# Kernel tuning notes

Hardware: AMD Instinct MI355X
Metric: run time of the kernel (lower is better)

The kernel has to match this reference:

```python
import jax, jax.numpy as jnp
import numpy as np

MUL0, MUL1 = 32, 16          # multiplicities of 0e and 1o in irreps_node
RBF, HID = 16, 64
O1 = MUL0 * MUL0             # path 0e x 0e -> 0e
O2 = O1 + MUL0 * MUL1        # path 0e x 1o -> 1o
O3 = O2 + MUL1 * MUL1        # path 1o x 0e -> 1o
WNUMEL = O3 + MUL1 * MUL0    # path 1o x 1o -> 0e  => 2304 total
C_PATH = 1.0 / np.sqrt(MUL0 + MUL1).astype(np.float32)  # per-output fan-in norm
C_110 = 1.0 / np.sqrt(3.0)   # CG factor for 1o x 1o -> 0e (component norm)


def setup_inputs() -> dict:
    key = jax.random.key(0)
    ks = jax.random.split(key, 16)
    N, E = 50000, 200000
    x = jax.random.normal(ks[0], (N, MUL0 + 3 * MUL1), jnp.float32)
    edge_src = jax.random.randint(ks[1], (E,), 0, N)
    edge_dst = jax.random.randint(ks[2], (E,), 0, N)
    edge_sh = jax.random.normal(ks[3], (E, 4), jnp.float32)
    edge_rbf = jax.random.uniform(ks[4], (E, RBF), jnp.float32)
    # RadialMLP params (fan-in scaled init)
    w1 = jax.random.normal(ks[5], (RBF, HID), jnp.float32) / np.sqrt(RBF)
    b1 = jnp.zeros((HID,), jnp.float32)
    w2 = jax.random.normal(ks[6], (HID, HID), jnp.float32) / np.sqrt(HID)
    b2 = jnp.zeros((HID,), jnp.float32)
    w3 = jax.random.normal(ks[7], (HID, WNUMEL), jnp.float32) / np.sqrt(HID)
    b3 = jnp.zeros((WNUMEL,), jnp.float32)
    # o3.Linear weights (per-irrep mixing, fan-in normalization folded in)
    ws_self = jax.random.normal(ks[8], (MUL0, MUL0), jnp.float32) / np.sqrt(MUL0)
    wv_self = jax.random.normal(ks[9], (MUL1, MUL1), jnp.float32) / np.sqrt(MUL1)
    ws_out = jax.random.normal(ks[10], (MUL0, MUL0), jnp.float32) / np.sqrt(MUL0)
    wv_out = jax.random.normal(ks[11], (MUL1, MUL1), jnp.float32) / np.sqrt(MUL1)
    return {"x": x, "edge_src": edge_src, "edge_dst": edge_dst,
            "edge_sh": edge_sh, "edge_rbf": edge_rbf,
            "w1": w1, "b1": b1, "w2": w2, "b2": b2, "w3": w3, "b3": b3,
            "ws_self": ws_self, "wv_self": wv_self,
            "ws_out": ws_out, "wv_out": wv_out}


def _irrep_linear(x, ws, wv):
    # per-irrep mixing of '32x0e + 16x1o' features; x: [N, 80]
    n = x.shape[0]
    s = x[:, :MUL0] @ ws                                     # [N, 32]
    v = jnp.einsum('nid,io->nod', x[:, MUL0:].reshape(n, MUL1, 3), wv)
    return jnp.concatenate([s, v.reshape(n, 3 * MUL1)], axis=-1)


def reference(x, edge_src, edge_dst, edge_sh, edge_rbf,
              w1, b1, w2, b2, w3, b3, ws_self, wv_self, ws_out, wv_out):
    N = x.shape[0]
    E = edge_rbf.shape[0]
    # radial MLP -> per-edge TP weights [E, 2304]
    h = jax.nn.silu(edge_rbf @ w1 + b1)
    h = jax.nn.silu(h @ w2 + b2)
    W = h @ w3 + b3
    W1 = W[:, :O1].reshape(E, MUL0, MUL0)      # 0e x 0e -> 0e
    W2 = W[:, O1:O2].reshape(E, MUL0, MUL1)    # 0e x 1o -> 1o
    W3 = W[:, O2:O3].reshape(E, MUL1, MUL1)    # 1o x 0e -> 1o
    W4 = W[:, O3:].reshape(E, MUL1, MUL0)      # 1o x 1o -> 0e
    # gather source node features per edge
    xs = x[edge_src, :MUL0]                                   # [E, 32]
    xv = x[edge_src, MUL0:].reshape(E, MUL1, 3)               # [E, 16, 3]
    sh_s = edge_sh[:, 0]                                      # [E]
    sh_v = edge_sh[:, 1:4]                                    # [E, 3]
    # CG tensor product paths
    out_s = jnp.einsum('ei,eio->eo', xs * sh_s[:, None], W1)
    out_s = out_s + C_110 * jnp.einsum('eid,ed,eio->eo', xv, sh_v, W4)
    out_v = jnp.einsum('ei,ed,eio->eod', xs, sh_v, W2)
    out_v = out_v + jnp.einsum('eid,eio->eod', xv * sh_s[:, None, None], W3)
    m = C_PATH * jnp.concatenate([out_s, out_v.reshape(E, 3 * MUL1)], axis=-1)
    # scatter-add + degree normalize
    agg = jax.ops.segment_sum(m, edge_dst, num_segments=N)
    deg = jax.ops.segment_sum(jnp.ones((E,), x.dtype), edge_dst, num_segments=N)
    agg = agg / jnp.maximum(deg, 1.0)[:, None]
    return _irrep_linear(x, ws_self, wv_self) + _irrep_linear(agg, ws_out, wv_out)
```

## Files before the change

### kernel.cpp

```cpp
#include <hip/hip_runtime.h>
#include <math.h>

#define MUL0    32
#define MUL1    16
#define RBFD    16
#define HIDD    64
#define OFF1    1024
#define OFF2    1536
#define OFF3    1792
#define WNUMEL  2304
#define FDIM    80
#define CPATH   0.14433756729740643f
#define C110    0.57735026918962576f

#define TE       160
#define NTHREADS 320
#define NCT      144

#define W3B_ELEMS (NCT*2*64*8)
#define W1B_ELEMS (4*64*8)
#define W2B_ELEMS (4*2*64*8)

typedef float          f32x4   __attribute__((ext_vector_type(4)));
typedef short          short8  __attribute__((ext_vector_type(8)));
typedef short          short4v __attribute__((ext_vector_type(4)));
typedef unsigned short u16;

__device__ __forceinline__ float silu(float v) {
    return v / (1.0f + __expf(-v));
}
__device__ __forceinline__ u16 f2bf(float f) {
    unsigned int u = __float_as_uint(f);
    u += 0x7fffu + ((u >> 16) & 1u);
    return (u16)(u >> 16);
}
__device__ __forceinline__ float bf2f(u16 s) {
    return __uint_as_float(((unsigned int)s) << 16);
}
__device__ __forceinline__ f32x4 cvt4(short4v s) {
    f32x4 r;
    r[0] = bf2f((u16)s[0]); r[1] = bf2f((u16)s[1]);
    r[2] = bf2f((u16)s[2]); r[3] = bf2f((u16)s[3]);
    return r;
}
__device__ __forceinline__ f32x4 mfma16(short8 a, short8 b, f32x4 c) {
    return __builtin_amdgcn_mfma_f32_16x16x32_bf16(a, b, c, 0, 0, 0);
}

__global__ void k_prep(const float* __restrict__ w3,
                       const float* __restrict__ w1,
                       const float* __restrict__ w2,
                       u16* __restrict__ w3b,
                       u16* __restrict__ w1b,
                       u16* __restrict__ w2b) {
    int idx = blockIdx.x * 256 + threadIdx.x;
    if (idx < W3B_ELEMS) {
        int j  = idx & 7;
        int l  = (idx >> 3) & 63;
        int kh = (idx >> 9) & 1;
        int ct = idx >> 10;
        int k = kh * 32 + 8 * (l >> 4) + j;
        int c = ct * 16 + (l & 15);
        w3b[idx] = f2bf(w3[k * WNUMEL + c]);
        return;
    }
    idx -= W3B_ELEMS;
    if (idx < W1B_ELEMS) {
        int j  = idx & 7;
        int l  = (idx >> 3) & 63;
        int ct = idx >> 9;
        int k = 8 * (l >> 4) + j;
        int c = ct * 16 + (l & 15);
        w1b[idx] = (k < RBFD) ? f2bf(w1[k * HIDD + c]) : (u16)0;
        return;
    }
    idx -= W1B_ELEMS;
    if (idx < W2B_ELEMS) {
        int j  = idx & 7;
        int l  = (idx >> 3) & 63;
        int kh = (idx >> 9) & 1;
        int ct = idx >> 10;
        int k = kh * 32 + 8 * (l >> 4) + j;
        int c = ct * 16 + (l & 15);
        w2b[idx] = f2bf(w2[k * HIDD + c]);
    }
}

__global__ __launch_bounds__(320)
void k_edge(const float* __restrict__ x,
            const int*   __restrict__ esrc,
            const int*   __restrict__ edst,
            const float* __restrict__ esh,
            const float* __restrict__ erbf,
            const u16*   __restrict__ w1b,
            const float* __restrict__ b1,
            const u16*   __restrict__ w2b,
            const float* __restrict__ b2,
            const u16*   __restrict__ w3b,
            const float* __restrict__ b3,
            float* __restrict__ agg,
            float* __restrict__ deg)
{
    __shared__ alignas(16) unsigned char smem[54016];
    u16*   S     = (u16*)smem;
    float* s_b3  = (float*)(smem + 40960);
    float* s_sh  = (float*)(smem + 50176);
    int*   s_src = (int*)(smem + 52736);
    int*   s_dst = (int*)(smem + 53376);

    const int tid = threadIdx.x;
    const int eb  = blockIdx.x * TE;
    const int w   = tid >> 6;
    const int l   = tid & 63;
    const int lo  = l & 15;
    const int g   = l >> 4;

    if (tid < TE) {
        s_src[tid] = esrc[eb + tid];
        s_dst[tid] = edst[eb + tid];
    }
    for (int idx = tid; idx < TE * 4; idx += NTHREADS)
        s_sh[idx] = esh[eb * 4 + idx];

    float cb1[4], cb2[4];
    #pragma unroll
    for (int ct = 0; ct < 4; ++ct) {
        cb1[ct] = b1[ct * 16 + lo];
        cb2[ct] = b2[ct * 16 + lo];
    }

    const short8* W1B = (const short8*)w1b;
    const short8* W2B = (const short8*)w2b;

    #pragma unroll
    for (int gr = 0; gr < 2; ++gr) {
        const int e0 = 32 * w + 16 * gr;
        short8 ar = {0, 0, 0, 0, 0, 0, 0, 0};
        if (g < 2) {
            const float* rp = erbf + (size_t)(eb + e0 + lo) * RBFD + 8 * g;
            f32x4 r0 = *(const f32x4*)rp;
            f32x4 r1 = *(const f32x4*)(rp + 4);
            ar[0] = f2bf(r0[0]); ar[1] = f2bf(r0[1]);
            ar[2] = f2bf(r0[2]); ar[3] = f2bf(r0[3]);
            ar[4] = f2bf(r1[0]); ar[5] = f2bf(r1[1]);
            ar[6] = f2bf(r1[2]); ar[7] = f2bf(r1[3]);
        }
        #pragma unroll
        for (int ct = 0; ct < 4; ++ct) {
            f32x4 t = {cb1[ct], cb1[ct], cb1[ct], cb1[ct]};
            t = mfma16(ar, W1B[ct * 64 + l], t);
            #pragma unroll
            for (int r = 0; r < 4; ++r)
                S[(e0 + 4 * g + r) * 72 + ct * 16 + lo] = f2bf(silu(t[r]));
        }
    }

    #pragma unroll
    for (int gr = 0; gr < 2; ++gr) {
        const int e0 = 32 * w + 16 * gr;
        short8 a0 = *(const short8*)&S[(e0 + lo) * 72 + 0  + 8 * g];
        short8 a1 = *(const short8*)&S[(e0 + lo) * 72 + 32 + 8 * g];
        #pragma unroll
        for (int ct = 0; ct < 4; ++ct) {
            f32x4 t = {cb2[ct], cb2[ct], cb2[ct], cb2[ct]};
            t = mfma16(a0, W2B[(ct * 2 + 0) * 64 + l], t);
            t = mfma16(a1, W2B[(ct * 2 + 1) * 64 + l], t);
            #pragma unroll
            for (int r = 0; r < 4; ++r)
                S[(e0 + 4 * g + r) * 72 + ct * 16 + lo] = f2bf(silu(t[r]));
        }
    }

    short8 a[2][2];
    #pragma unroll
    for (int rt = 0; rt < 2; ++rt) {
        const int e0 = 32 * w + 16 * rt;
        a[rt][0] = *(const short8*)&S[(e0 + lo) * 72 + 0  + 8 * g];
        a[rt][1] = *(const short8*)&S[(e0 + lo) * 72 + 32 + 8 * g];
    }
    __syncthreads();

    if (tid < TE) {
        const int el = tid, grp = el >> 4, e16 = el & 15;
        const float sh0 = s_sh[el * 4 + 0];
        const float sh1 = s_sh[el * 4 + 1];
        const float sh2 = s_sh[el * 4 + 2];
        const float sh3 = s_sh[el * 4 + 3];
        const float* xrow = x + (size_t)s_src[el] * FDIM;
        u16* fsB = S + grp * 768 + e16;
        u16* xsB = S + 7680  + grp * 512 + e16;
        u16* xvB = S + 12800 + grp * 768 + e16;
        #pragma unroll
        for (int v = 0; v < 8; ++v) {
            f32x4 x4 = *(const f32x4*)(xrow + 4 * v);
            #pragma unroll
            for (int c2 = 0; c2 < 4; ++c2) {
                int i = 4 * v + c2;
                fsB[i * 16] = f2bf(x4[c2] * sh0);
                xsB[i * 16] = f2bf(x4[c2]);
            }
        }
        float buf[48];
        #pragma unroll
        for (int v = 0; v < 12; ++v) {
            f32x4 t4 = *(const f32x4*)(xrow + MUL0 + 4 * v);
            buf[4*v] = t4[0]; buf[4*v+1] = t4[1];
            buf[4*v+2] = t4[2]; buf[4*v+3] = t4[3];
        }
        #pragma unroll
        for (int i = 0; i < 16; ++i) {
            float v0 = buf[3*i], v1 = buf[3*i+1], v2 = buf[3*i+2];
            xvB[(0  + i) * 16] = f2bf(v0 * sh0);
            xvB[(16 + i) * 16] = f2bf(v1 * sh0);
            xvB[(32 + i) * 16] = f2bf(v2 * sh0);
            fsB[(32 + i) * 16] = f2bf(C110 * (v0 * sh1 + v1 * sh2 + v2 * sh3));
        }
    } else {
        for (int idx = tid - TE; idx < WNUMEL; idx += NTHREADS - TE)
            s_b3[idx] = b3[idx];
    }
    __syncthreads();

    const short8* WB = (const short8*)w3b;
    f32x4 acc[2][6];
    #pragma unroll
    for (int rt = 0; rt < 2; ++rt)
        #pragma unroll
        for (int p = 0; p < 6; ++p)
            acc[rt][p] = (f32x4){0.f, 0.f, 0.f, 0.f};

    for (int i = 0; i < 32; ++i) {
        if ((i & 3) == 0 && i) __builtin_amdgcn_s_barrier();
        short8 b0a = WB[(4*i + 0) * 64 + l];
        short8 b0b = WB[(4*i + 1) * 64 + l];
        short8 b1a = WB[(4*i + 2) * 64 + l];
        short8 b1b = WB[(4*i + 3) * 64 + l];
        short8 b2a = WB[(128 + 2*i) * 64 + l];
        short8 b2b = WB[(129 + 2*i) * 64 + l];
        float bs0 = s_b3[(2*i)     * 16 + lo];
        float bs1 = s_b3[(2*i + 1) * 16 + lo];
        float bs2 = s_b3[(64 + i)  * 16 + lo];
        #pragma unroll
        for (int rt = 0; rt < 2; ++rt) {
            const int fb = 2 * w + rt;
            f32x4 t0 = {bs0, bs0, bs0, bs0};
            t0 = mfma16(a[rt][0], b0a, t0); t0 = mfma16(a[rt][1], b0b, t0);
            f32x4 t1 = {bs1, bs1, bs1, bs1};
            t1 = mfma16(a[rt][0], b1a, t1); t1 = mfma16(a[rt][1], b1b, t1);
            f32x4 t2 = {bs2, bs2, bs2, bs2};
            t2 = mfma16(a[rt][0], b2a, t2); t2 = mfma16(a[rt][1], b2b, t2);
            f32x4 f1 = cvt4(*(const short4v*)&S[fb * 768 + i * 16 + 4 * g]);
            f32x4 f2 = cvt4(*(const short4v*)&S[7680 + fb * 512 + i * 16 + 4 * g]);
            acc[rt][0] += f1 * t0;
            acc[rt][1] += f1 * t1;
            acc[rt][2] += f2 * t2;
        }
    }
    for (int i = 0; i < 16; ++i) {
        if ((i & 3) == 0) __builtin_amdgcn_s_barrier();
        short8 b4a0 = WB[(224 + 4*i) * 64 + l];
        short8 b4a1 = WB[(225 + 4*i) * 64 + l];
        short8 b4b0 = WB[(226 + 4*i) * 64 + l];
        short8 b4b1 = WB[(227 + 4*i) * 64 + l];
        short8 b3a  = WB[(192 + 2*i) * 64 + l];
        short8 b3b  = WB[(193 + 2*i) * 64 + l];
        float bs0 = s_b3[(112 + 2*i) * 16 + lo];
        float bs1 = s_b3[(113 + 2*i) * 16 + lo];
        float bs2 = s_b3[(96 + i)    * 16 + lo];
        #pragma unroll
        for (int rt = 0; rt < 2; ++rt) {
            const int fb = 2 * w + rt;
            f32x4 t4a = {bs0, bs0, bs0, bs0};
            t4a = mfma16(a[rt][0], b4a0, t4a); t4a = mfma16(a[rt][1], b4a1, t4a);
            f32x4 t4b = {bs1, bs1, bs1, bs1};
            t4b = mfma16(a[rt][0], b4b0, t4b); t4b = mfma16(a[rt][1], b4b1, t4b);
            f32x4 t3 = {bs2, bs2, bs2, bs2};
            t3 = mfma16(a[rt][0], b3a, t3); t3 = mfma16(a[rt][1], b3b, t3);
            f32x4 f4 = cvt4(*(const short4v*)&S[fb * 768 + (32 + i) * 16 + 4 * g]);
            f32x4 v0 = cvt4(*(const short4v*)&S[12800 + fb * 768 + (0  + i) * 16 + 4 * g]);
            f32x4 v1 = cvt4(*(const short4v*)&S[12800 + fb * 768 + (16 + i) * 16 + 4 * g]);
            f32x4 v2 = cvt4(*(const short4v*)&S[12800 + fb * 768 + (32 + i) * 16 + 4 * g]);
            acc[rt][0] += f4 * t4a;
            acc[rt][1] += f4 * t4b;
            acc[rt][3] += v0 * t3;
            acc[rt][4] += v1 * t3;
            acc[rt][5] += v2 * t3;
        }
    }

    #pragma unroll
    for (int rt = 0; rt < 2; ++rt) {
        #pragma unroll
        for (int r = 0; r < 4; ++r) {
            const int e_loc = 32 * w + 16 * rt + 4 * g + r;
            float* row = agg + (size_t)s_dst[e_loc] * FDIM;
            atomicAdd(row + lo,      CPATH * acc[rt][0][r]);
            atomicAdd(row + 16 + lo, CPATH * acc[rt][1][r]);
            float sv0 = s_sh[e_loc * 4 + 1];
            float sv1 = s_sh[e_loc * 4 + 2];
            float sv2 = s_sh[e_loc * 4 + 3];
            atomicAdd(row + MUL0 + lo * 3 + 0, CPATH * (sv0 * acc[rt][2][r] + acc[rt][3][r]));
            atomicAdd(row + MUL0 + lo * 3 + 1, CPATH * (sv1 * acc[rt][2][r] + acc[rt][4][r]));
            atomicAdd(row + MUL0 + lo * 3 + 2, CPATH * (sv2 * acc[rt][2][r] + acc[rt][5][r]));
        }
    }
    if (tid < TE) atomicAdd(deg + s_dst[tid], 1.0f);
}

#define NPB 16
__global__ __launch_bounds__(256)
void k_node(const float* __restrict__ x,
            const float* __restrict__ deg,
            const float* __restrict__ ws_self,
            const float* __restrict__ wv_self,
            const float* __restrict__ ws_out,
            const float* __restrict__ wv_out,
            float* __restrict__ out)
{
    __shared__ float s_x[NPB][81];
    __shared__ float s_a[NPB][81];
    __shared__ float s_inv[NPB];

    const int tid = threadIdx.x;
    const int n0  = blockIdx.x * NPB;

    if (tid < NPB) s_inv[tid] = 1.0f / fmaxf(deg[n0 + tid], 1.0f);
    const float* xb = x   + (size_t)n0 * FDIM;
    const float* ab = out + (size_t)n0 * FDIM;
    for (int idx = tid; idx < NPB * FDIM; idx += 256) {
        int nl = idx / FDIM, jj = idx - nl * FDIM;
        s_x[nl][jj] = xb[idx];
        s_a[nl][jj] = ab[idx];
    }
    __syncthreads();

    const int j  = tid & 15;
    const int nl = tid >> 4;
    const float inv = s_inv[nl];
    float* orow = out + (size_t)(n0 + nl) * FDIM;

    float s1s = 0.f, s1a = 0.f, s2s = 0.f, s2a = 0.f;
    #pragma unroll
    for (int i = 0; i < MUL0; ++i) {
        float xs = s_x[nl][i], as = s_a[nl][i];
        s1s += xs * ws_self[i * MUL0 + j];
        s1a += as * ws_out [i * MUL0 + j];
        s2s += xs * ws_self[i * MUL0 + j + 16];
        s2a += as * ws_out [i * MUL0 + j + 16];
    }
    orow[j]      = s1s + inv * s1a;
    orow[j + 16] = s2s + inv * s2a;

    float vs[3] = {0.f, 0.f, 0.f}, va[3] = {0.f, 0.f, 0.f};
    #pragma unroll
    for (int i = 0; i < MUL1; ++i) {
        float wsf = wv_self[i * MUL1 + j];
        float wof = wv_out [i * MUL1 + j];
        #pragma unroll
        for (int d = 0; d < 3; ++d) {
            vs[d] += s_x[nl][MUL0 + 3 * i + d] * wsf;
            va[d] += s_a[nl][MUL0 + 3 * i + d] * wof;
        }
    }
    #pragma unroll
    for (int d = 0; d < 3; ++d)
        orow[MUL0 + j * 3 + d] = vs[d] + inv * va[d];
}

extern "C" void kernel_launch(void* const* d_in, const int* in_sizes, int n_in,
                              void* d_out, int out_size, void* d_ws, size_t ws_size,
                              hipStream_t stream)
{
    const float* x       = (const float*)d_in[0];
    const int*   esrc    = (const int*)  d_in[1];
    const int*   edst    = (const int*)  d_in[2];
    const float* esh     = (const float*)d_in[3];
    const float* erbf    = (const float*)d_in[4];
    const float* w1      = (const float*)d_in[5];
    const float* b1      = (const float*)d_in[6];
    const float* w2      = (const float*)d_in[7];
    const float* b2      = (const float*)d_in[8];
    const float* w3      = (const float*)d_in[9];
    const float* b3      = (const float*)d_in[10];
    const float* ws_self = (const float*)d_in[11];
    const float* wv_self = (const float*)d_in[12];
    const float* ws_out  = (const float*)d_in[13];
    const float* wv_out  = (const float*)d_in[14];

    const int N = in_sizes[0] / FDIM;
    const int E = in_sizes[1];

    char* wsp = (char*)d_ws;
    float* deg = (float*)wsp;
    size_t off = ((size_t)N * sizeof(float) + 255) & ~(size_t)255;
    u16* w3b = (u16*)(wsp + off);
    off += ((size_t)W3B_ELEMS * 2 + 255) & ~(size_t)255;
    u16* w1b = (u16*)(wsp + off);
    off += ((size_t)W1B_ELEMS * 2 + 255) & ~(size_t)255;
    u16* w2b = (u16*)(wsp + off);

    hipMemsetAsync(d_out, 0, (size_t)out_size * sizeof(float), stream);
    hipMemsetAsync(deg, 0, (size_t)N * sizeof(float), stream);

    k_prep<<<(W3B_ELEMS + W1B_ELEMS + W2B_ELEMS + 255) / 256, 256, 0, stream>>>(
        w3, w1, w2, w3b, w1b, w2b);

    k_edge<<<E / TE, NTHREADS, 0, stream>>>(
        x, esrc, edst, esh, erbf, w1b, b1, w2b, b2, w3b, b3,
        (float*)d_out, deg);

    k_node<<<N / NPB, 256, 0, stream>>>(
        x, deg, ws_self, wv_self, ws_out, wv_out, (float*)d_out);
}
```

Measured before the change: 281.1 us.

## Stream W3 weight tiles into LDS with triple-buffered async loads, enlarge edge tile

Repacks the bf16 W3 weights into per-iteration chunks of six MFMA tiles and streams them into shared memory with global_load_lds, triple-buffered and guarded by waitcnt plus barrier. Previously each wave loaded the same weight fragments directly from global memory. The two loops are merged into one 48-iteration loop, the block grows to 192 edges / 384 threads, and tail edges get bounds checks. This should cut redundant global weight traffic and overlap loads with MFMA work, at the cost of more LDS (about 81KB per block, which may limit occupancy) and one barrier per iteration.

```diff
diff --git a/kernel.cpp b/kernel.cpp
--- a/kernel.cpp
+++ b/kernel.cpp
@@ -5,21 +5,28 @@
 #define MUL1    16
 #define RBFD    16
 #define HIDD    64
-#define OFF1    1024
-#define OFF2    1536
-#define OFF3    1792
 #define WNUMEL  2304
 #define FDIM    80
 #define CPATH   0.14433756729740643f
 #define C110    0.57735026918962576f
 
-#define TE       160
-#define NTHREADS 320
-#define NCT      144
-
-#define W3B_ELEMS (NCT*2*64*8)
+#define TE       192
+#define NTHREADS 384
+#define NITER    48
+#define CHUNK_B  6144
+
+#define W3N_ELEMS (NITER*6*512)
 #define W1B_ELEMS (4*64*8)
 #define W2B_ELEMS (4*2*64*8)
+
+#define XS_U16   9216
+#define XV_U16   15360
+#define BBUF_B   49152
+#define B3_B     67584
+#define SH_B     76800
+#define SRC_B    79872
+#define DST_B    80640
+#define SMEM_B   81408
 
 typedef float          f32x4   __attribute__((ext_vector_type(4)));
 typedef short          short8  __attribute__((ext_vector_type(8)));
@@ -46,29 +53,37 @@
 __device__ __forceinline__ f32x4 mfma16(short8 a, short8 b, f32x4 c) {
     return __builtin_amdgcn_mfma_f32_16x16x32_bf16(a, b, c, 0, 0, 0);
 }
+__device__ __forceinline__ void gload16(const void* g, void* l) {
+    __builtin_amdgcn_global_load_lds(
+        (const __attribute__((address_space(1))) unsigned int*)g,
+        (__attribute__((address_space(3))) unsigned int*)l, 16, 0, 0);
+}
+
+__device__ __forceinline__ int tile_of(int t, int pair) {
+    if (t < 32) return (pair == 0) ? 2*t : (pair == 1) ? 2*t + 1 : 64 + t;
+    int tt = t - 32;
+    return (pair == 0) ? 112 + 2*tt : (pair == 1) ? 113 + 2*tt : 96 + tt;
+}
 
 __global__ void k_prep(const float* __restrict__ w3,
                        const float* __restrict__ w1,
                        const float* __restrict__ w2,
-                       u16* __restrict__ w3b,
+                       u16* __restrict__ w3n,
                        u16* __restrict__ w1b,
                        u16* __restrict__ w2b) {
     int idx = blockIdx.x * 256 + threadIdx.x;
-    if (idx < W3B_ELEMS) {
-        int j  = idx & 7;
-        int l  = (idx >> 3) & 63;
-        int kh = (idx >> 9) & 1;
-        int ct = idx >> 10;
+    if (idx < W3N_ELEMS) {
+        int j = idx & 7, l = (idx >> 3) & 63, f = idx >> 9;
+        int t = f / 6, s = f - 6 * t, pair = s >> 1, kh = s & 1;
+        int tile = tile_of(t, pair);
         int k = kh * 32 + 8 * (l >> 4) + j;
-        int c = ct * 16 + (l & 15);
-        w3b[idx] = f2bf(w3[k * WNUMEL + c]);
+        int c = tile * 16 + (l & 15);
+        w3n[idx] = f2bf(w3[k * WNUMEL + c]);
         return;
     }
-    idx -= W3B_ELEMS;
+    idx -= W3N_ELEMS;
     if (idx < W1B_ELEMS) {
-        int j  = idx & 7;
-        int l  = (idx >> 3) & 63;
-        int ct = idx >> 9;
+        int j = idx & 7, l = (idx >> 3) & 63, ct = idx >> 9;
         int k = 8 * (l >> 4) + j;
         int c = ct * 16 + (l & 15);
         w1b[idx] = (k < RBFD) ? f2bf(w1[k * HIDD + c]) : (u16)0;
@@ -76,17 +91,14 @@
     }
     idx -= W1B_ELEMS;
     if (idx < W2B_ELEMS) {
-        int j  = idx & 7;
-        int l  = (idx >> 3) & 63;
-        int kh = (idx >> 9) & 1;
-        int ct = idx >> 10;
+        int j = idx & 7, l = (idx >> 3) & 63, kh = (idx >> 9) & 1, ct = idx >> 10;
         int k = kh * 32 + 8 * (l >> 4) + j;
         int c = ct * 16 + (l & 15);
         w2b[idx] = f2bf(w2[k * HIDD + c]);
     }
 }
 
-__global__ __launch_bounds__(320)
+__global__ __launch_bounds__(NTHREADS, 3)
 void k_edge(const float* __restrict__ x,
             const int*   __restrict__ esrc,
             const int*   __restrict__ edst,
@@ -96,17 +108,18 @@
             const float* __restrict__ b1,
             const u16*   __restrict__ w2b,
             const float* __restrict__ b2,
-            const u16*   __restrict__ w3b,
+            const u16*   __restrict__ w3n,
             const float* __restrict__ b3,
             float* __restrict__ agg,
-            float* __restrict__ deg)
+            float* __restrict__ deg,
+            int E)
 {
-    __shared__ alignas(16) unsigned char smem[54016];
+    __shared__ alignas(16) unsigned char smem[SMEM_B];
     u16*   S     = (u16*)smem;
-    float* s_b3  = (float*)(smem + 40960);
-    float* s_sh  = (float*)(smem + 50176);
-    int*   s_src = (int*)(smem + 52736);
-    int*   s_dst = (int*)(smem + 53376);
+    float* s_b3  = (float*)(smem + B3_B);
+    float* s_sh  = (float*)(smem + SH_B);
+    int*   s_src = (int*)(smem + SRC_B);
+    int*   s_dst = (int*)(smem + DST_B);
 
     const int tid = threadIdx.x;
     const int eb  = blockIdx.x * TE;
@@ -116,34 +129,32 @@
     const int g   = l >> 4;
 
     if (tid < TE) {
-        s_src[tid] = esrc[eb + tid];
-        s_dst[tid] = edst[eb + tid];
-    }
-    for (int idx = tid; idx < TE * 4; idx += NTHREADS)
-        s_sh[idx] = esh[eb * 4 + idx];
+        int eg = eb + tid;
+        s_src[tid] = (eg < E) ? esrc[eg] : 0;
+        s_dst[tid] = (eg < E) ? edst[eg] : 0;
+    }
+    for (int idx = tid; idx < TE * 4; idx += NTHREADS) {
+        long eg4 = (long)eb * 4 + idx;
+        s_sh[idx] = (eg4 < (long)E * 4) ? esh[eg4] : 0.0f;
+    }
+    __syncthreads();
 
     float cb1[4], cb2[4];
     #pragma unroll
-    for (int ct = 0; ct < 4; ++ct) {
-        cb1[ct] = b1[ct * 16 + lo];
-        cb2[ct] = b2[ct * 16 + lo];
-    }
-
+    for (int ct = 0; ct < 4; ++ct) { cb1[ct] = b1[ct*16 + lo]; cb2[ct] = b2[ct*16 + lo]; }
     const short8* W1B = (const short8*)w1b;
     const short8* W2B = (const short8*)w2b;
 
     #pragma unroll
     for (int gr = 0; gr < 2; ++gr) {
         const int e0 = 32 * w + 16 * gr;
-        short8 ar = {0, 0, 0, 0, 0, 0, 0, 0};
-        if (g < 2) {
+        short8 ar = {0,0,0,0,0,0,0,0};
+        if (g < 2 && (eb + e0 + lo) < E) {
             const float* rp = erbf + (size_t)(eb + e0 + lo) * RBFD + 8 * g;
             f32x4 r0 = *(const f32x4*)rp;
             f32x4 r1 = *(const f32x4*)(rp + 4);
-            ar[0] = f2bf(r0[0]); ar[1] = f2bf(r0[1]);
-            ar[2] = f2bf(r0[2]); ar[3] = f2bf(r0[3]);
-            ar[4] = f2bf(r1[0]); ar[5] = f2bf(r1[1]);
-            ar[6] = f2bf(r1[2]); ar[7] = f2bf(r1[3]);
+            ar[0]=f2bf(r0[0]); ar[1]=f2bf(r0[1]); ar[2]=f2bf(r0[2]); ar[3]=f2bf(r0[3]);
+            ar[4]=f2bf(r1[0]); ar[5]=f2bf(r1[1]); ar[6]=f2bf(r1[2]); ar[7]=f2bf(r1[3]);
         }
         #pragma unroll
         for (int ct = 0; ct < 4; ++ct) {
@@ -151,45 +162,43 @@
             t = mfma16(ar, W1B[ct * 64 + l], t);
             #pragma unroll
             for (int r = 0; r < 4; ++r)
-                S[(e0 + 4 * g + r) * 72 + ct * 16 + lo] = f2bf(silu(t[r]));
-        }
-    }
-
+                S[(e0 + 4*g + r) * 72 + ct*16 + lo] = f2bf(silu(t[r]));
+        }
+    }
     #pragma unroll
     for (int gr = 0; gr < 2; ++gr) {
         const int e0 = 32 * w + 16 * gr;
-        short8 a0 = *(const short8*)&S[(e0 + lo) * 72 + 0  + 8 * g];
-        short8 a1 = *(const short8*)&S[(e0 + lo) * 72 + 32 + 8 * g];
+        short8 a0 = *(const short8*)&S[(e0 + lo) * 72 + 0  + 8*g];
+        short8 a1 = *(const short8*)&S[(e0 + lo) * 72 + 32 + 8*g];
         #pragma unroll
         for (int ct = 0; ct < 4; ++ct) {
             f32x4 t = {cb2[ct], cb2[ct], cb2[ct], cb2[ct]};
-            t = mfma16(a0, W2B[(ct * 2 + 0) * 64 + l], t);
-            t = mfma16(a1, W2B[(ct * 2 + 1) * 64 + l], t);
+            t = mfma16(a0, W2B[(ct*2 + 0) * 64 + l], t);
+            t = mfma16(a1, W2B[(ct*2 + 1) * 64 + l], t);
             #pragma unroll
             for (int r = 0; r < 4; ++r)
-                S[(e0 + 4 * g + r) * 72 + ct * 16 + lo] = f2bf(silu(t[r]));
-        }
-    }
-
+                S[(e0 + 4*g + r) * 72 + ct*16 + lo] = f2bf(silu(t[r]));
+        }
+    }
     short8 a[2][2];
     #pragma unroll
     for (int rt = 0; rt < 2; ++rt) {
         const int e0 = 32 * w + 16 * rt;
-        a[rt][0] = *(const short8*)&S[(e0 + lo) * 72 + 0  + 8 * g];
-        a[rt][1] = *(const short8*)&S[(e0 + lo) * 72 + 32 + 8 * g];
+        a[rt][0] = *(const short8*)&S[(e0 + lo) * 72 + 0  + 8*g];
+        a[rt][1] = *(const short8*)&S[(e0 + lo) * 72 + 32 + 8*g];
     }
     __syncthreads();
 
     if (tid < TE) {
         const int el = tid, grp = el >> 4, e16 = el & 15;
-        const float sh0 = s_sh[el * 4 + 0];
-        const float sh1 = s_sh[el * 4 + 1];
-        const float sh2 = s_sh[el * 4 + 2];
-        const float sh3 = s_sh[el * 4 + 3];
+        const float sh0 = s_sh[el*4 + 0];
+        const float sh1 = s_sh[el*4 + 1];
+        const float sh2 = s_sh[el*4 + 2];
+        const float sh3 = s_sh[el*4 + 3];
         const float* xrow = x + (size_t)s_src[el] * FDIM;
         u16* fsB = S + grp * 768 + e16;
-        u16* xsB = S + 7680  + grp * 512 + e16;
-        u16* xvB = S + 12800 + grp * 768 + e16;
+        u16* xsB = S + XS_U16 + grp * 512 + e16;
+        u16* xvB = S + XV_U16 + grp * 768 + e16;
         #pragma unroll
         for (int v = 0; v < 8; ++v) {
             f32x4 x4 = *(const f32x4*)(xrow + 4 * v);
@@ -204,8 +213,7 @@
         #pragma unroll
         for (int v = 0; v < 12; ++v) {
             f32x4 t4 = *(const f32x4*)(xrow + MUL0 + 4 * v);
-            buf[4*v] = t4[0]; buf[4*v+1] = t4[1];
-            buf[4*v+2] = t4[2]; buf[4*v+3] = t4[3];
+            buf[4*v]=t4[0]; buf[4*v+1]=t4[1]; buf[4*v+2]=t4[2]; buf[4*v+3]=t4[3];
         }
         #pragma unroll
         for (int i = 0; i < 16; ++i) {
@@ -213,98 +221,92 @@
             xvB[(0  + i) * 16] = f2bf(v0 * sh0);
             xvB[(16 + i) * 16] = f2bf(v1 * sh0);
             xvB[(32 + i) * 16] = f2bf(v2 * sh0);
-            fsB[(32 + i) * 16] = f2bf(C110 * (v0 * sh1 + v1 * sh2 + v2 * sh3));
+            fsB[(32 + i) * 16] = f2bf(C110 * (v0*sh1 + v1*sh2 + v2*sh3));
         }
     } else {
-        for (int idx = tid - TE; idx < WNUMEL; idx += NTHREADS - TE)
-            s_b3[idx] = b3[idx];
+        for (int idx = tid - TE; idx < WNUMEL; idx += NTHREADS - TE) {
+            int t = idx / 48, r = idx - 48 * t, pair = r >> 4, lo16 = r & 15;
+            s_b3[idx] = b3[tile_of(t, pair) * 16 + lo16];
+        }
     }
     __syncthreads();
 
-    const short8* WB = (const short8*)w3b;
+    gload16((const char*)w3n + tid * 16, smem + BBUF_B + tid * 16);
+
     f32x4 acc[2][6];
     #pragma unroll
     for (int rt = 0; rt < 2; ++rt)
         #pragma unroll
-        for (int p = 0; p < 6; ++p)
-            acc[rt][p] = (f32x4){0.f, 0.f, 0.f, 0.f};
-
-    for (int i = 0; i < 32; ++i) {
-        if ((i & 3) == 0 && i) __builtin_amdgcn_s_barrier();
-        short8 b0a = WB[(4*i + 0) * 64 + l];
-        short8 b0b = WB[(4*i + 1) * 64 + l];
-        short8 b1a = WB[(4*i + 2) * 64 + l];
-        short8 b1b = WB[(4*i + 3) * 64 + l];
-        short8 b2a = WB[(128 + 2*i) * 64 + l];
-        short8 b2b = WB[(129 + 2*i) * 64 + l];
-        float bs0 = s_b3[(2*i)     * 16 + lo];
-        float bs1 = s_b3[(2*i + 1) * 16 + lo];
-        float bs2 = s_b3[(64 + i)  * 16 + lo];
+        for (int p = 0; p < 6; ++p) acc[rt][p] = (f32x4){0.f,0.f,0.f,0.f};
+
+    const char* gp = (const char*)w3n + CHUNK_B + tid * 16;
+    int bo_r = 0, bo_w = CHUNK_B;
+
+    for (int t = 0; t < NITER; ++t) {
+        if (t < NITER - 1) {
+            gload16(gp, smem + BBUF_B + bo_w + tid * 16);
+            gp += CHUNK_B;
+            asm volatile("s_waitcnt vmcnt(1)" ::: "memory");
+        } else {
+            asm volatile("s_waitcnt vmcnt(0)" ::: "memory");
+        }
+        __builtin_amdgcn_s_barrier();
+
+        const u16* BC = (const u16*)(smem + BBUF_B + bo_r);
+        short8 bA0 = *(const short8*)(BC + 0*512 + l*8);
+        short8 bA1 = *(const short8*)(BC + 1*512 + l*8);
+        short8 bB0 = *(const short8*)(BC + 2*512 + l*8);
+        short8 bB1 = *(const short8*)(BC + 3*512 + l*8);
+        short8 bC0 = *(const short8*)(BC + 4*512 + l*8);
+        short8 bC1 = *(const short8*)(BC + 5*512 + l*8);
+        float bs0 = s_b3[t*48 + lo];
+        float bs1 = s_b3[t*48 + 16 + lo];
+        float bs2 = s_b3[t*48 + 32 + lo];
+
         #pragma unroll
         for (int rt = 0; rt < 2; ++rt) {
             const int fb = 2 * w + rt;
-            f32x4 t0 = {bs0, bs0, bs0, bs0};
-            t0 = mfma16(a[rt][0], b0a, t0); t0 = mfma16(a[rt][1], b0b, t0);
-            f32x4 t1 = {bs1, bs1, bs1, bs1};
-            t1 = mfma16(a[rt][0], b1a, t1); t1 = mfma16(a[rt][1], b1b, t1);
-            f32x4 t2 = {bs2, bs2, bs2, bs2};
-            t2 = mfma16(a[rt][0], b2a, t2); t2 = mfma16(a[rt][1], b2b, t2);
-            f32x4 f1 = cvt4(*(const short4v*)&S[fb * 768 + i * 16 + 4 * g]);
-            f32x4 f2 = cvt4(*(const short4v*)&S[7680 + fb * 512 + i * 16 + 4 * g]);
-            acc[rt][0] += f1 * t0;
-            acc[rt][1] += f1 * t1;
-            acc[rt][2] += f2 * t2;
-        }
-    }
-    for (int i = 0; i < 16; ++i) {
-        if ((i & 3) == 0) __builtin_amdgcn_s_barrier();
-        short8 b4a0 = WB[(224 + 4*i) * 64 + l];
-        short8 b4a1 = WB[(225 + 4*i) * 64 + l];
-        short8 b4b0 = WB[(226 + 4*i) * 64 + l];
-        short8 b4b1 = WB[(227 + 4*i) * 64 + l];
-        short8 b3a  = WB[(192 + 2*i) * 64 + l];
-        short8 b3b  = WB[(193 + 2*i) * 64 + l];
-        float bs0 = s_b3[(112 + 2*i) * 16 + lo];
-        float bs1 = s_b3[(113 + 2*i) * 16 + lo];
-        float bs2 = s_b3[(96 + i)    * 16 + lo];
-        #pragma unroll
-        for (int rt = 0; rt < 2; ++rt) {
-            const int fb = 2 * w + rt;
-            f32x4 t4a = {bs0, bs0, bs0, bs0};
-            t4a = mfma16(a[rt][0], b4a0, t4a); t4a = mfma16(a[rt][1], b4a1, t4a);
-            f32x4 t4b = {bs1, bs1, bs1, bs1};
-            t4b = mfma16(a[rt][0], b4b0, t4b); t4b = mfma16(a[rt][1], b4b1, t4b);
-            f32x4 t3 = {bs2, bs2, bs2, bs2};
-            t3 = mfma16(a[rt][0], b3a, t3); t3 = mfma16(a[rt][1], b3b, t3);
-            f32x4 f4 = cvt4(*(const short4v*)&S[fb * 768 + (32 + i) * 16 + 4 * g]);
-            f32x4 v0 = cvt4(*(const short4v*)&S[12800 + fb * 768 + (0  + i) * 16 + 4 * g]);
-            f32x4 v1 = cvt4(*(const short4v*)&S[12800 + fb * 768 + (16 + i) * 16 + 4 * g]);
-            f32x4 v2 = cvt4(*(const short4v*)&S[12800 + fb * 768 + (32 + i) * 16 + 4 * g]);
-            acc[rt][0] += f4 * t4a;
-            acc[rt][1] += f4 * t4b;
-            acc[rt][3] += v0 * t3;
-            acc[rt][4] += v1 * t3;
-            acc[rt][5] += v2 * t3;
-        }
+            f32x4 tA = {bs0, bs0, bs0, bs0};
+            tA = mfma16(a[rt][0], bA0, tA); tA = mfma16(a[rt][1], bA1, tA);
+            f32x4 tB = {bs1, bs1, bs1, bs1};
+            tB = mfma16(a[rt][0], bB0, tB); tB = mfma16(a[rt][1], bB1, tB);
+            f32x4 tC = {bs2, bs2, bs2, bs2};
+            tC = mfma16(a[rt][0], bC0, tC); tC = mfma16(a[rt][1], bC1, tC);
+
+            f32x4 fA = cvt4(*(const short4v*)&S[fb*768 + t*16 + 4*g]);
+            acc[rt][0] += fA * tA;
+            acc[rt][1] += fA * tB;
+            if (t < 32) {
+                f32x4 fx = cvt4(*(const short4v*)&S[XS_U16 + fb*512 + t*16 + 4*g]);
+                acc[rt][2] += fx * tC;
+            } else {
+                const int i = t - 32;
+                acc[rt][3] += cvt4(*(const short4v*)&S[XV_U16 + fb*768 + (0 +i)*16 + 4*g]) * tC;
+                acc[rt][4] += cvt4(*(const short4v*)&S[XV_U16 + fb*768 + (16+i)*16 + 4*g]) * tC;
+                acc[rt][5] += cvt4(*(const short4v*)&S[XV_U16 + fb*768 + (32+i)*16 + 4*g]) * tC;
+            }
+        }
+        bo_r = (bo_r == 2*CHUNK_B) ? 0 : bo_r + CHUNK_B;
+        bo_w = (bo_w == 2*CHUNK_B) ? 0 : bo_w + CHUNK_B;
     }
 
     #pragma unroll
     for (int rt = 0; rt < 2; ++rt) {
         #pragma unroll
         for (int r = 0; r < 4; ++r) {
-            const int e_loc = 32 * w + 16 * rt + 4 * g + r;
+            const int e_loc = 32*w + 16*rt + 4*g + r;
             float* row = agg + (size_t)s_dst[e_loc] * FDIM;
             atomicAdd(row + lo,      CPATH * acc[rt][0][r]);
             atomicAdd(row + 16 + lo, CPATH * acc[rt][1][r]);
-            float sv0 = s_sh[e_loc * 4 + 1];
-            float sv1 = s_sh[e_loc * 4 + 2];
-            float sv2 = s_sh[e_loc * 4 + 3];
-            atomicAdd(row + MUL0 + lo * 3 + 0, CPATH * (sv0 * acc[rt][2][r] + acc[rt][3][r]));
-            atomicAdd(row + MUL0 + lo * 3 + 1, CPATH * (sv1 * acc[rt][2][r] + acc[rt][4][r]));
-            atomicAdd(row + MUL0 + lo * 3 + 2, CPATH * (sv2 * acc[rt][2][r] + acc[rt][5][r]));
-        }
-    }
-    if (tid < TE) atomicAdd(deg + s_dst[tid], 1.0f);
+            float sv0 = s_sh[e_loc*4 + 1];
+            float sv1 = s_sh[e_loc*4 + 2];
+            float sv2 = s_sh[e_loc*4 + 3];
+            atomicAdd(row + MUL0 + lo*3 + 0, CPATH * (sv0*acc[rt][2][r] + acc[rt][3][r]));
+            atomicAdd(row + MUL0 + lo*3 + 1, CPATH * (sv1*acc[rt][2][r] + acc[rt][4][r]));
+            atomicAdd(row + MUL0 + lo*3 + 2, CPATH * (sv2*acc[rt][2][r] + acc[rt][5][r]));
+        }
+    }
+    if (tid < TE && (eb + tid) < E) atomicAdd(deg + s_dst[tid], 1.0f);
 }
 
 #define NPB 16
@@ -351,20 +353,20 @@
     orow[j]      = s1s + inv * s1a;
     orow[j + 16] = s2s + inv * s2a;
 
-    float vs[3] = {0.f, 0.f, 0.f}, va[3] = {0.f, 0.f, 0.f};
+    float vs[3] = {0.f,0.f,0.f}, va[3] = {0.f,0.f,0.f};
     #pragma unroll
     for (int i = 0; i < MUL1; ++i) {
         float wsf = wv_self[i * MUL1 + j];
         float wof = wv_out [i * MUL1 + j];
         #pragma unroll
         for (int d = 0; d < 3; ++d) {
-            vs[d] += s_x[nl][MUL0 + 3 * i + d] * wsf;
-            va[d] += s_a[nl][MUL0 + 3 * i + d] * wof;
+            vs[d] += s_x[nl][MUL0 + 3*i + d] * wsf;
+            va[d] += s_a[nl][MUL0 + 3*i + d] * wof;
         }
     }
     #pragma unroll
     for (int d = 0; d < 3; ++d)
-        orow[MUL0 + j * 3 + d] = vs[d] + inv * va[d];
+        orow[MUL0 + j*3 + d] = vs[d] + inv * va[d];
 }
 
 extern "C" void kernel_launch(void* const* d_in, const int* in_sizes, int n_in,
@@ -393,8 +395,8 @@
     char* wsp = (char*)d_ws;
     float* deg = (float*)wsp;
     size_t off = ((size_t)N * sizeof(float) + 255) & ~(size_t)255;
-    u16* w3b = (u16*)(wsp + off);
-    off += ((size_t)W3B_ELEMS * 2 + 255) & ~(size_t)255;
+    u16* w3n = (u16*)(wsp + off);
+    off += ((size_t)W3N_ELEMS * 2 + 255) & ~(size_t)255;
     u16* w1b = (u16*)(wsp + off);
     off += ((size_t)W1B_ELEMS * 2 + 255) & ~(size_t)255;
     u16* w2b = (u16*)(wsp + off);
@@ -402,12 +404,13 @@
     hipMemsetAsync(d_out, 0, (size_t)out_size * sizeof(float), stream);
     hipMemsetAsync(deg, 0, (size_t)N * sizeof(float), stream);
 
-    k_prep<<<(W3B_ELEMS + W1B_ELEMS + W2B_ELEMS + 255) / 256, 256, 0, stream>>>(
-        w3, w1, w2, w3b, w1b, w2b);
-
-    k_edge<<<E / TE, NTHREADS, 0, stream>>>(
-        x, esrc, edst, esh, erbf, w1b, b1, w2b, b2, w3b, b3,
-        (float*)d_out, deg);
+    k_prep<<<(W3N_ELEMS + W1B_ELEMS + W2B_ELEMS + 255) / 256, 256, 0, stream>>>(
+        w3, w1, w2, w3n, w1b, w2b);
+
+    const int nblk = (E + TE - 1) / TE;
+    k_edge<<<nblk, NTHREADS, 0, stream>>>(
+        x, esrc, edst, esh, erbf, w1b, b1, w2b, b2, w3n, b3,
+        (float*)d_out, deg, E);
 
     k_node<<<N / NPB, 256, 0, stream>>>(
         x, deg, ws_self, wv_self, ws_out, wv_out, (float*)d_out);
```

Result: slower. 320.3 us (+14.0%).
